# Kernel optimization log

Measured on AMD Instinct MI355X. Metric: run time of the kernel, lower is better.

The kernel has to match this reference:

```python
import jax, jax.numpy as jnp
import numpy as np

D_MODEL = 512; D_STATE = 64; D_CONV = 4; EXPAND = 2; HEADDIM = 64
D_INNER = EXPAND * D_MODEL          # 1024
NHEADS = D_INNER // HEADDIM         # 16
D_IN_PROJ = 2 * D_INNER + 2 * D_STATE + NHEADS  # z, xBC, dt
CONV_DIM = D_INNER + 2 * D_STATE
BETA = 0.5
BATCH = 8; SEQLEN = 1024
EPS_LN = 1e-12; EPS_RMS = 1e-5


def layernorm(x, w, b, eps=EPS_LN):
    mu = jnp.mean(x, axis=-1, keepdims=True)
    var = jnp.var(x, axis=-1, keepdims=True)
    return (x - mu) * jax.lax.rsqrt(var + eps) * w + b


def causal_dw_conv(x, w, b):
    # x: (b, l, c); w: (c, d_conv) depthwise; causal left-pad d_conv-1
    xt = jnp.transpose(x, (0, 2, 1))                 # (b, c, l)
    k = w[:, None, :]                                # (c, 1, d_conv)
    y = jax.lax.conv_general_dilated(
        xt, k, window_strides=(1,), padding=[(D_CONV - 1, 0)],
        feature_group_count=CONV_DIM,
        dimension_numbers=('NCH', 'OIH', 'NCH'))
    return jnp.transpose(y, (0, 2, 1)) + b


def ssd(x, dt, A, Bm, Cm, Dp):
    # x: (b,l,h,p)  dt: (b,l,h)  A: (h)  Bm,Cm: (b,l,n)  Dp: (h)
    dA = jnp.exp(dt * A)  # (b,l,h) decay per step

    def step(h, inp):
        dA_t, dt_t, B_t, C_t, x_t = inp
        # h: (b, heads, p, n)
        h = h * dA_t[:, :, None, None] + jnp.einsum('bh,bn,bhp->bhpn', dt_t, B_t, x_t)
        y = jnp.einsum('bhpn,bn->bhp', h, C_t)
        return h, y

    init = jnp.zeros((x.shape[0], NHEADS, HEADDIM, D_STATE), x.dtype)
    xs = (jnp.moveaxis(dA, 1, 0), jnp.moveaxis(dt, 1, 0),
          jnp.moveaxis(Bm, 1, 0), jnp.moveaxis(Cm, 1, 0), jnp.moveaxis(x, 1, 0))
    _, ys = jax.lax.scan(step, init, xs)
    y = jnp.moveaxis(ys, 0, 1)           # (b,l,h,p)
    return y + x * Dp[None, None, :, None]


def mamba2(u, in_proj_w, conv_w, conv_b, dt_bias, A_log, Dp, norm_w, out_proj_w):
    zxbcdt = u @ in_proj_w.T                                   # (b,l,D_IN_PROJ)
    z, xBC, dt = jnp.split(zxbcdt, [D_INNER, D_INNER + CONV_DIM], axis=-1)
    dt = jax.nn.softplus(dt + dt_bias)                          # (b,l,h)
    xBC = jax.nn.silu(causal_dw_conv(xBC, conv_w, conv_b))
    x, Bm, Cm = jnp.split(xBC, [D_INNER, D_INNER + D_STATE], axis=-1)
    x = x.reshape(x.shape[0], x.shape[1], NHEADS, HEADDIM)
    A = -jnp.exp(A_log)
    y = ssd(x, dt, A, Bm, Cm, Dp)
    y = y.reshape(y.shape[0], y.shape[1], D_INNER)
    g = y * jax.nn.silu(z)                                      # gated RMSNorm
    g = g * jax.lax.rsqrt(jnp.mean(g * g, axis=-1, keepdims=True) + EPS_RMS) * norm_w
    return g @ out_proj_w.T


def ffn(x, w1, b1, w2, b2, lnw, lnb):
    h = jax.nn.gelu(x @ w1.T + b1, approximate=False)
    h = h @ w2.T + b2
    return layernorm(h + x, lnw, lnb)


def setup_inputs() -> dict:
    key = jax.random.key(0)
    ks = jax.random.split(key, 12)
    item_emb = jax.random.normal(ks[0], (BATCH, SEQLEN, D_MODEL), jnp.float32)
    item_idx = jnp.zeros((BATCH, SEQLEN), jnp.int32)          # single sequence per row
    flip_index = jnp.arange(SEQLEN - 1, -1, -1, dtype=jnp.int64)
    s = 0.02
    in_proj_w = jax.random.normal(ks[1], (D_IN_PROJ, D_MODEL), jnp.float32) * s
    conv_w = jax.random.uniform(ks[2], (CONV_DIM, D_CONV), jnp.float32, -0.5, 0.5)
    conv_b = jnp.zeros((CONV_DIM,), jnp.float32)
    # dt_bias = inverse softplus of dt ~ U[1e-3, 0.1] in log space (mamba init)
    dt = jnp.exp(jax.random.uniform(ks[3], (NHEADS,), jnp.float32,
                                    np.log(1e-3), np.log(0.1)))
    dt_bias = dt + jnp.log(-jnp.expm1(-dt))
    A_log = jnp.log(jax.random.uniform(ks[4], (NHEADS,), jnp.float32, 1.0, 16.0))
    Dp = jnp.ones((NHEADS,), jnp.float32)
    norm_w = jnp.ones((D_INNER,), jnp.float32)
    out_proj_w = jax.random.normal(ks[5], (D_MODEL, D_INNER), jnp.float32) * s
    ln_w = jnp.ones((D_MODEL,), jnp.float32); ln_b = jnp.zeros((D_MODEL,), jnp.float32)
    ffn_w1 = jax.random.normal(ks[6], (4 * D_MODEL, D_MODEL), jnp.float32) * s
    ffn_b1 = jnp.zeros((4 * D_MODEL,), jnp.float32)
    ffn_w2 = jax.random.normal(ks[7], (D_MODEL, 4 * D_MODEL), jnp.float32) * s
    ffn_b2 = jnp.zeros((D_MODEL,), jnp.float32)
    ffn_ln_w = jnp.ones((D_MODEL,), jnp.float32); ffn_ln_b = jnp.zeros((D_MODEL,), jnp.float32)
    return dict(item_emb=item_emb, item_idx=item_idx, flip_index=flip_index,
                in_proj_w=in_proj_w, conv_w=conv_w, conv_b=conv_b, dt_bias=dt_bias,
                A_log=A_log, Dp=Dp, norm_w=norm_w, out_proj_w=out_proj_w,
                ln_w=ln_w, ln_b=ln_b, ffn_w1=ffn_w1, ffn_b1=ffn_b1,
                ffn_w2=ffn_w2, ffn_b2=ffn_b2, ffn_ln_w=ffn_ln_w, ffn_ln_b=ffn_ln_b)


def reference(item_emb, item_idx, flip_index, in_proj_w, conv_w, conv_b, dt_bias,
              A_log, Dp, norm_w, out_proj_w, ln_w, ln_b,
              ffn_w1, ffn_b1, ffn_w2, ffn_b2, ffn_ln_w, ffn_ln_b):
    # item_idx (seq_idx) is all-zeros -> no state resets; dropout is eval-mode identity.
    params = (in_proj_w, conv_w, conv_b, dt_bias, A_log, Dp, norm_w, out_proj_w)
    fwd = mamba2(item_emb, *params)
    bwd = mamba2(item_emb[:, flip_index, :], *params)   # shared weights, as in source
    h = fwd + bwd * BETA + item_emb
    h = layernorm(h, ln_w, ln_b)
    return ffn(h, ffn_w1, ffn_b1, ffn_w2, ffn_b2, ffn_ln_w, ffn_ln_b)
```

## Files before the change

kernel.cpp:

```cpp
#include <hip/hip_runtime.h>
#include <math.h>

#define SEQ     1024
#define NBATCH  8
#define NTOK    8192
#define DMODEL  512
#define DINNER  1024
#define NHEADS  16
#define DPROJ   2192
#define DPROJP  2304
#define CONVDIM 1152
#define DFFN    2048

typedef short bf16x8 __attribute__((ext_vector_type(8)));
typedef float f32x4  __attribute__((ext_vector_type(4)));

__device__ inline unsigned short f2bf(float f) {
  union { float f; unsigned int u; } v; v.f = f;
  unsigned int u = v.u;
  return (unsigned short)((u + 0x7FFFu + ((u >> 16) & 1u)) >> 16);
}
__device__ inline float bf2f(unsigned short s) {
  union { unsigned int u; float f; } v; v.u = ((unsigned int)s) << 16;
  return v.f;
}

#define GLDS16(g, l)                                                         \
  __builtin_amdgcn_global_load_lds(                                          \
      (const __attribute__((address_space(1))) unsigned int*)(g),            \
      (__attribute__((address_space(3))) unsigned int*)(l), 16, 0, 0)

__global__ __launch_bounds__(256) void cvt_bf16(const float* __restrict__ s,
                                                unsigned short* __restrict__ d, int n) {
  int i = blockIdx.x * 256 + threadIdx.x;
  if (i < n) d[i] = f2bf(s[i]);
}

__global__ __launch_bounds__(256) void cvt_bf16_pad(const float* __restrict__ s,
                                                    unsigned short* __restrict__ d,
                                                    int realrows, int cols, int padrows) {
  int i = blockIdx.x * 256 + threadIdx.x;
  if (i < padrows * cols) {
    int r = i / cols;
    d[i] = (r < realrows) ? f2bf(s[i]) : (unsigned short)0;
  }
}

template <int MODE>
__global__ __launch_bounds__(256)
void gemm_bt(const unsigned short* __restrict__ A, const unsigned short* __restrict__ B,
             void* __restrict__ Cout, const float* __restrict__ bias,
             float* __restrict__ aux, int Ksub, int lda, int Nreal, size_t zstrideC) {
  __shared__ unsigned short sA[2][128 * 32];
  __shared__ unsigned short sB[2][128 * 32];
  const int tid = threadIdx.x;
  const int bx = blockIdx.x, by = blockIdx.y, bz = blockIdx.z;
  const int lane = tid & 63;
  const int wave = tid >> 6;
  const int wm = wave >> 1, wn = wave & 1;
  const int arow = tid >> 2;
  const int acol = (tid & 3) << 3;

  const unsigned short* pA = A + (size_t)(by * 128 + arow) * lda + bz * Ksub + acol;
  const unsigned short* pB = B + (size_t)(bx * 128 + arow) * lda + bz * Ksub + acol;
  const size_t stride64 = (size_t)64 * lda;
  char* sAw[2] = { (char*)&sA[0][0] + wave * 1024, (char*)&sA[1][0] + wave * 1024 };
  char* sBw[2] = { (char*)&sB[0][0] + wave * 1024, (char*)&sB[1][0] + wave * 1024 };

  f32x4 acc[4][4];
#pragma unroll
  for (int i = 0; i < 4; i++)
#pragma unroll
    for (int j = 0; j < 4; j++) { f32x4 z = {0.f, 0.f, 0.f, 0.f}; acc[i][j] = z; }

  GLDS16(pA, sAw[0]);
  GLDS16(pA + stride64, sAw[0] + 4096);
  GLDS16(pB, sBw[0]);
  GLDS16(pB + stride64, sBw[0] + 4096);
  pA += 32; pB += 32;
  __syncthreads();

  const int lrow = lane & 15;
  const int lkq = (lane >> 4) << 3;
  int cur = 0;
  for (int k0 = 0; k0 < Ksub; k0 += 32) {
    if (k0 + 32 < Ksub) {
      const int nxt = cur ^ 1;
      GLDS16(pA, sAw[nxt]);
      GLDS16(pA + stride64, sAw[nxt] + 4096);
      GLDS16(pB, sBw[nxt]);
      GLDS16(pB + stride64, sBw[nxt] + 4096);
      pA += 32; pB += 32;
    }
    bf16x8 af[4], bfr[4];
#pragma unroll
    for (int mi = 0; mi < 4; mi++)
      af[mi] = *(const bf16x8*)&sA[cur][(wm * 64 + mi * 16 + lrow) * 32 + lkq];
#pragma unroll
    for (int ni = 0; ni < 4; ni++)
      bfr[ni] = *(const bf16x8*)&sB[cur][(wn * 64 + ni * 16 + lrow) * 32 + lkq];
#pragma unroll
    for (int mi = 0; mi < 4; mi++)
#pragma unroll
      for (int ni = 0; ni < 4; ni++)
        acc[mi][ni] = __builtin_amdgcn_mfma_f32_16x16x32_bf16(af[mi], bfr[ni], acc[mi][ni], 0, 0, 0);
    __syncthreads();
    cur ^= 1;
  }

  const int row0 = by * 128 + wm * 64;
  const int col0 = bx * 128 + wn * 64;
  float* outf = (float*)Cout;
  unsigned short* outp16 = (unsigned short*)Cout + (size_t)bz * zstrideC;
#pragma unroll
  for (int mi = 0; mi < 4; mi++) {
#pragma unroll
    for (int ni = 0; ni < 4; ni++) {
      const int col = col0 + ni * 16 + lrow;
      if (col < Nreal) {
        const float bval = (MODE == 0 || MODE == 1) && bias ? bias[col] : 0.f;
#pragma unroll
        for (int r = 0; r < 4; r++) {
          const int row = row0 + mi * 16 + ((lane >> 4) << 2) + r;
          float v = acc[mi][ni][r] + bval;
          if (MODE == 1) {
            float g = 0.5f * v * (1.f + erff(v * 0.7071067811865476f));
            ((unsigned short*)Cout)[(size_t)row * Nreal + col] = f2bf(g);
          } else if (MODE == 2) {
            ((unsigned short*)Cout)[(size_t)row * Nreal + col] = f2bf(v);
            if (col >= 2176) aux[(size_t)row * 16 + (col - 2176)] = v;
          } else if (MODE == 3) {
            outp16[(size_t)row * Nreal + col] = f2bf(v);
          } else {
            outf[(size_t)row * Nreal + col] = v;
          }
        }
      }
    }
  }
}

__global__ __launch_bounds__(256)
void dt_softplus(const float* __restrict__ zdt, const float* __restrict__ dt_bias,
                 float* __restrict__ dtf, float* __restrict__ dtb) {
  int i = blockIdx.x * 256 + threadIdx.x;
  int dir = i >> 17;
  int rem = i & 131071;
  int row = rem >> 10;
  int t = rem & 1023;
  int b = row >> 4, h = row & 15;
  int srow = (b << 10) + (dir ? (1023 - t) : t);
  float v = zdt[(size_t)srow * 16 + h] + dt_bias[h];
  float dt = (v > 20.f) ? v : log1pf(expf(v));
  (dir ? dtb : dtf)[(row << 10) + t] = dt;
}

__global__ __launch_bounds__(256)
void conv_silu_bf(const unsigned short* __restrict__ zxb, const float* __restrict__ cw,
                  const float* __restrict__ cb,
                  unsigned short* __restrict__ xcf, unsigned short* __restrict__ xcb) {
  const int tid = threadIdx.x;
  const int c = blockIdx.x * 128 + (tid & 127);
  const int b = blockIdx.y;
  const int seg = blockIdx.z * 2 + (tid >> 7);
  const int t0 = seg << 5;
  const float w0 = cw[c * 4 + 0], w1 = cw[c * 4 + 1], w2 = cw[c * 4 + 2], w3 = cw[c * 4 + 3];
  const float bias = cb[c];
  const unsigned short* src = zxb + (size_t)(b << 10) * DPROJ + DINNER + c;
  unsigned short* dstf = xcf + (size_t)(b << 10) * CONVDIM + c;
  unsigned short* dstb = xcb + (size_t)(b << 10) * CONVDIM + c;
  float r0 = 0.f, r1 = 0.f, r2 = 0.f;
  if (t0 >= 3) {
    r0 = bf2f(src[(size_t)(t0 - 3) * DPROJ]);
    r1 = bf2f(src[(size_t)(t0 - 2) * DPROJ]);
    r2 = bf2f(src[(size_t)(t0 - 1) * DPROJ]);
  }
  for (int s = t0; s < t0 + 32; s++) {
    float x = bf2f(src[(size_t)s * DPROJ]);
    float vf = bias + w0 * r0 + w1 * r1 + w2 * r2 + w3 * x;
    dstf[(size_t)s * CONVDIM] = f2bf(vf / (1.f + expf(-vf)));
    int tp = 1026 - s;
    if (tp <= 1023) {
      float vb = bias + w0 * x + w1 * r2 + w2 * r1 + w3 * r0;
      dstb[(size_t)tp * CONVDIM] = f2bf(vb / (1.f + expf(-vb)));
    }
    r0 = r1; r1 = r2; r2 = x;
  }
  if (seg == 31) {
    float v2 = bias + w1 * r2 + w2 * r1 + w3 * r0;
    float v1 = bias + w2 * r2 + w3 * r1;
    float v0 = bias + w3 * r2;
    dstb[(size_t)2 * CONVDIM] = f2bf(v2 / (1.f + expf(-v2)));
    dstb[(size_t)1 * CONVDIM] = f2bf(v1 / (1.f + expf(-v1)));
    dstb[0] = f2bf(v0 / (1.f + expf(-v0)));
  }
}

__global__ __launch_bounds__(512)
void ssd_chunk(const unsigned short* __restrict__ xcf, const unsigned short* __restrict__ xcb,
               const float* __restrict__ dtf, const float* __restrict__ dtb,
               const float* __restrict__ A_log, const float* __restrict__ Dp,
               unsigned short* __restrict__ yf, unsigned short* __restrict__ yb) {
  const int blk = blockIdx.x;
  const int dir = blk >> 7;
  const int b = (blk >> 4) & 7;
  const int h = blk & 15;
  const unsigned short* xc = dir ? xcb : xcf;
  const float* dts = (dir ? dtb : dtf) + ((size_t)((b << 4) + h) << 10);
  unsigned short* yo = dir ? yb : yf;
  const float A = -expf(A_log[h]);
  const float Dh = Dp[h];
  const int tid = threadIdx.x;
  const int lane = tid & 63;
  const int w = tid >> 6;
  const int wm = w >> 1;
  const int wn = w & 1;
  const int lrow = lane & 15;
  const int quad = lane >> 4;
  const int lk8 = quad << 3;
  const int bS = b << 10;

  __shared__ unsigned short Cb[2][64 * 72];
  __shared__ unsigned short Bb[2][64 * 72];
  __shared__ unsigned short Xt[2][64 * 72];
  __shared__ unsigned short Bt[2][64 * 72];
  __shared__ unsigned short Hb[2][64 * 72];
  __shared__ unsigned short Mb[64 * 72];
  __shared__ float sdt_all[1024];
  __shared__ float Lv_all[16][64];
  __shared__ float ev_all[16][64];
  __shared__ float wv_all[16][64];
  __shared__ float dtot_all[16];

  const unsigned short* bcrow = xc + (size_t)(bS + (tid >> 3)) * CONVDIM + (tid & 7) * 8;
  const int pr = tid & 31;
  const int sg = tid >> 5;
  const unsigned short* trow = xc + (size_t)(bS + sg * 4) * CONVDIM;

  uint4 vb, vc;
  unsigned int xv[4], bv[4];

  vb = *(const uint4*)(bcrow + 1024);
  vc = *(const uint4*)(bcrow + 1088);
  {
    const unsigned short* tp = trow;
#pragma unroll
    for (int k = 0; k < 4; k++) {
      xv[k] = *(const unsigned int*)(tp + h * 64 + pr * 2);
      bv[k] = *(const unsigned int*)(tp + 1024 + pr * 2);
      tp += CONVDIM;
    }
  }

  *(float2*)&sdt_all[tid * 2] = *(const float2*)(dts + tid * 2);
  {
    uint4 z; z.x = 0u; z.y = 0u; z.z = 0u; z.w = 0u;
    *(uint4*)&Hb[0][(tid >> 3) * 72 + (tid & 7) * 8] = z;
  }
  __syncthreads();

#pragma unroll
  for (int r = 0; r < 2; r++) {
    const int c = w * 2 + r;
    float dtl = sdt_all[c * 64 + lane];
    float v = dtl;
#pragma unroll
    for (int off = 1; off < 64; off <<= 1) {
      float o = __shfl_up(v, off);
      if (lane >= off) v += o;
    }
    const float Lv = A * v;
    const float LL = __shfl(Lv, 63);
    Lv_all[c][lane] = Lv;
    ev_all[c][lane] = expf(Lv);
    wv_all[c][lane] = dtl * expf(LL - Lv);
    if (lane == 0) dtot_all[c] = expf(LL);
  }
  __syncthreads();

  auto stage_write = [&](int buf, int c) {
    *(uint4*)&Bb[buf][(tid >> 3) * 72 + (tid & 7) * 8] = vb;
    *(uint4*)&Cb[buf][(tid >> 3) * 72 + (tid & 7) * 8] = vc;
    unsigned short x0[4], x1[4], b0[4], b1[4];
#pragma unroll
    for (int k = 0; k < 4; k++) {
      float ws = wv_all[c][sg * 4 + k];
      x0[k] = (unsigned short)(xv[k] & 0xffff);
      x1[k] = (unsigned short)(xv[k] >> 16);
      b0[k] = f2bf(bf2f((unsigned short)(bv[k] & 0xffff)) * ws);
      b1[k] = f2bf(bf2f((unsigned short)(bv[k] >> 16)) * ws);
    }
    *(uint2*)&Xt[buf][(pr * 2 + 0) * 72 + sg * 4] = *(const uint2*)x0;
    *(uint2*)&Xt[buf][(pr * 2 + 1) * 72 + sg * 4] = *(const uint2*)x1;
    *(uint2*)&Bt[buf][(pr * 2 + 0) * 72 + sg * 4] = *(const uint2*)b0;
    *(uint2*)&Bt[buf][(pr * 2 + 1) * 72 + sg * 4] = *(const uint2*)b1;
  };
  auto stage_load = [&](int c) {
    const unsigned short* rp = bcrow + (size_t)c * 64 * CONVDIM;
    vb = *(const uint4*)(rp + 1024);
    vc = *(const uint4*)(rp + 1088);
    const unsigned short* tp = trow + (size_t)c * 64 * CONVDIM;
#pragma unroll
    for (int k = 0; k < 4; k++) {
      xv[k] = *(const unsigned int*)(tp + h * 64 + pr * 2);
      bv[k] = *(const unsigned int*)(tp + 1024 + pr * 2);
      tp += CONVDIM;
    }
  };

  stage_write(0, 0);
  stage_load(1);
  __syncthreads();

  f32x4 hacc[2];
#pragma unroll
  for (int j = 0; j < 2; j++) { f32x4 z = {0.f, 0.f, 0.f, 0.f}; hacc[j] = z; }

  int cur = 0;
  for (int c = 0; c < 16; c++) {
    const int t0 = c << 6;

    f32x4 m1[2];
#pragma unroll
    for (int j = 0; j < 2; j++) { f32x4 z = {0.f, 0.f, 0.f, 0.f}; m1[j] = z; }
#pragma unroll
    for (int kq = 0; kq < 2; kq++) {
      bf16x8 af = *(const bf16x8*)&Cb[cur][(wm * 16 + lrow) * 72 + kq * 32 + lk8];
#pragma unroll
      for (int j = 0; j < 2; j++) {
        bf16x8 bf = *(const bf16x8*)&Bb[cur][(wn * 32 + j * 16 + lrow) * 72 + kq * 32 + lk8];
        m1[j] = __builtin_amdgcn_mfma_f32_16x16x32_bf16(af, bf, m1[j], 0, 0, 0);
      }
    }
#pragma unroll
    for (int r = 0; r < 4; r++) {
      const int i = wm * 16 + quad * 4 + r;
      const float Li = Lv_all[c][i];
#pragma unroll
      for (int j = 0; j < 2; j++) {
        const int s = wn * 32 + j * 16 + lrow;
        const float Ls = Lv_all[c][s];
        const float ds = sdt_all[c * 64 + s];
        float val = (s <= i) ? m1[j][r] * expf(Li - Ls) * ds : 0.f;
        Mb[i * 72 + s] = f2bf(val);
      }
    }
    __syncthreads();

    f32x4 Y[2], T[2], S[2];
#pragma unroll
    for (int j = 0; j < 2; j++) {
      f32x4 z = {0.f, 0.f, 0.f, 0.f};
      Y[j] = z; T[j] = z; S[j] = z;
    }
#pragma unroll
    for (int kq = 0; kq < 2; kq++) {
      bf16x8 am = *(const bf16x8*)&Mb[(wm * 16 + lrow) * 72 + kq * 32 + lk8];
      bf16x8 ac = *(const bf16x8*)&Cb[cur][(wm * 16 + lrow) * 72 + kq * 32 + lk8];
      bf16x8 ax = *(const bf16x8*)&Xt[cur][(wm * 16 + lrow) * 72 + kq * 32 + lk8];
#pragma unroll
      for (int j = 0; j < 2; j++) {
        const int brow = (wn * 32 + j * 16 + lrow) * 72 + kq * 32 + lk8;
        bf16x8 bx = *(const bf16x8*)&Xt[cur][brow];
        bf16x8 bh = *(const bf16x8*)&Hb[cur][brow];
        bf16x8 bw = *(const bf16x8*)&Bt[cur][brow];
        Y[j] = __builtin_amdgcn_mfma_f32_16x16x32_bf16(am, bx, Y[j], 0, 0, 0);
        T[j] = __builtin_amdgcn_mfma_f32_16x16x32_bf16(ac, bh, T[j], 0, 0, 0);
        S[j] = __builtin_amdgcn_mfma_f32_16x16x32_bf16(ax, bw, S[j], 0, 0, 0);
      }
    }

    const float dtot = dtot_all[c];
#pragma unroll
    for (int r = 0; r < 4; r++) {
      const int i = wm * 16 + quad * 4 + r;
      const float ei = ev_all[c][i];
#pragma unroll
      for (int j = 0; j < 2; j++) {
        const int p = wn * 32 + j * 16 + lrow;
        float yv = Y[j][r] + ei * T[j][r] + Dh * bf2f(Xt[cur][p * 72 + i]);
        yo[(size_t)(bS + t0 + i) * DINNER + h * 64 + p] = f2bf(yv);
      }
    }
#pragma unroll
    for (int j = 0; j < 2; j++)
#pragma unroll
      for (int r = 0; r < 4; r++)
        hacc[j][r] = dtot * hacc[j][r] + S[j][r];

    const int nxt = cur ^ 1;
    if (c + 1 < 16) {
#pragma unroll
      for (int j = 0; j < 2; j++)
#pragma unroll
        for (int r = 0; r < 4; r++)
          Hb[nxt][(wm * 16 + quad * 4 + r) * 72 + wn * 32 + j * 16 + lrow] = f2bf(hacc[j][r]);
      stage_write(nxt, c + 1);
      if (c + 2 < 16) stage_load(c + 2);
    }
    __syncthreads();
    cur = nxt;
  }
}

__device__ inline float2 block_sum2_256(float a, float b) {
#pragma unroll
  for (int o = 32; o >= 1; o >>= 1) { a += __shfl_xor(a, o); b += __shfl_xor(b, o); }
  __shared__ float ra[4], rb[4];
  const int lane = threadIdx.x & 63, w = threadIdx.x >> 6;
  if (lane == 0) { ra[w] = a; rb[w] = b; }
  __syncthreads();
  float2 out;
  out.x = ra[0] + ra[1] + ra[2] + ra[3];
  out.y = rb[0] + rb[1] + rb[2] + rb[3];
  return out;
}

__global__ __launch_bounds__(256)
void gate_rms_comb(const unsigned short* __restrict__ yf, const unsigned short* __restrict__ yb,
                   const unsigned short* __restrict__ zxb, const float* __restrict__ nw,
                   unsigned short* __restrict__ comb) {
  const int bt = blockIdx.x;
  const int b = bt >> 10, t = bt & 1023;
  const int zrowb = (b << 10) + (1023 - t);
  const int tid = threadIdx.x;
  ushort4 yf4 = *(const ushort4*)(yf + (size_t)bt * DINNER + tid * 4);
  ushort4 yb4 = *(const ushort4*)(yb + (size_t)bt * DINNER + tid * 4);
  ushort4 zf4 = *(const ushort4*)(zxb + (size_t)bt * DPROJ + tid * 4);
  ushort4 zb4 = *(const ushort4*)(zxb + (size_t)zrowb * DPROJ + tid * 4);
  float gf[4], gb[4];
  {
    float z0 = bf2f(zf4.x), z1 = bf2f(zf4.y), z2 = bf2f(zf4.z), z3 = bf2f(zf4.w);
    gf[0] = bf2f(yf4.x) * (z0 / (1.f + expf(-z0)));
    gf[1] = bf2f(yf4.y) * (z1 / (1.f + expf(-z1)));
    gf[2] = bf2f(yf4.z) * (z2 / (1.f + expf(-z2)));
    gf[3] = bf2f(yf4.w) * (z3 / (1.f + expf(-z3)));
  }
  {
    float z0 = bf2f(zb4.x), z1 = bf2f(zb4.y), z2 = bf2f(zb4.z), z3 = bf2f(zb4.w);
    gb[0] = bf2f(yb4.x) * (z0 / (1.f + expf(-z0)));
    gb[1] = bf2f(yb4.y) * (z1 / (1.f + expf(-z1)));
    gb[2] = bf2f(yb4.z) * (z2 / (1.f + expf(-z2)));
    gb[3] = bf2f(yb4.w) * (z3 / (1.f + expf(-z3)));
  }
  float2 sr = block_sum2_256(gf[0]*gf[0] + gf[1]*gf[1] + gf[2]*gf[2] + gf[3]*gf[3],
                             gb[0]*gb[0] + gb[1]*gb[1] + gb[2]*gb[2] + gb[3]*gb[3]);
  float sf = rsqrtf(sr.x * (1.f / 1024.f) + 1e-5f);
  float sb = 0.5f * rsqrtf(sr.y * (1.f / 1024.f) + 1e-5f);
  float4 wv = *(const float4*)(nw + tid * 4);
  unsigned short* o = comb + (size_t)bt * DINNER + tid * 4;
  o[0] = f2bf((gf[0] * sf + gb[0] * sb) * wv.x);
  o[1] = f2bf((gf[1] * sf + gb[1] * sb) * wv.y);
  o[2] = f2bf((gf[2] * sf + gb[2] * sb) * wv.z);
  o[3] = f2bf((gf[3] * sf + gb[3] * sb) * wv.w);
}

__global__ __launch_bounds__(256)
void combine_ln(const unsigned short* __restrict__ mo, const float* __restrict__ u,
                const float* __restrict__ w, const float* __restrict__ bias,
                float* __restrict__ hln, unsigned short* __restrict__ hbf) {
  const int bt = blockIdx.x;
  const int tid = threadIdx.x;
  const float2 uu = *(const float2*)(u + (size_t)bt * DMODEL + tid * 2);
  float vx = uu.x, vy = uu.y;
#pragma unroll
  for (int z = 0; z < 4; z++) {
    ushort2 p = *(const ushort2*)(mo + (size_t)z * NTOK * DMODEL + (size_t)bt * DMODEL + tid * 2);
    vx += bf2f(p.x);
    vy += bf2f(p.y);
  }
  float2 sr = block_sum2_256(vx + vy, vx * vx + vy * vy);
  float mean = sr.x * (1.f / 512.f);
  float var = sr.y * (1.f / 512.f) - mean * mean;
  float inv = rsqrtf(var + 1e-12f);
  float2 wv = *(const float2*)(w + tid * 2);
  float2 bv = *(const float2*)(bias + tid * 2);
  float ox = (vx - mean) * inv * wv.x + bv.x;
  float oy = (vy - mean) * inv * wv.y + bv.y;
  *(float2*)(hln + (size_t)bt * DMODEL + tid * 2) = make_float2(ox, oy);
  hbf[(size_t)bt * DMODEL + tid * 2] = f2bf(ox);
  hbf[(size_t)bt * DMODEL + tid * 2 + 1] = f2bf(oy);
}

__global__ __launch_bounds__(256)
void final_ln(const unsigned short* __restrict__ f2, const float* __restrict__ b2,
              const float* __restrict__ hln,
              const float* __restrict__ w, const float* __restrict__ bias,
              float* __restrict__ outp) {
  const int bt = blockIdx.x;
  const int tid = threadIdx.x;
  const float2 bb = *(const float2*)(b2 + tid * 2);
  const float2 h = *(const float2*)(hln + (size_t)bt * DMODEL + tid * 2);
  float vx = bb.x + h.x;
  float vy = bb.y + h.y;
#pragma unroll
  for (int z = 0; z < 4; z++) {
    ushort2 p = *(const ushort2*)(f2 + (size_t)z * NTOK * DMODEL + (size_t)bt * DMODEL + tid * 2);
    vx += bf2f(p.x);
    vy += bf2f(p.y);
  }
  float2 sr = block_sum2_256(vx + vy, vx * vx + vy * vy);
  float mean = sr.x * (1.f / 512.f);
  float var = sr.y * (1.f / 512.f) - mean * mean;
  float inv = rsqrtf(var + 1e-12f);
  float2 wv = *(const float2*)(w + tid * 2);
  float2 bv = *(const float2*)(bias + tid * 2);
  *(float2*)(outp + (size_t)bt * DMODEL + tid * 2) =
      make_float2((vx - mean) * inv * wv.x + bv.x, (vy - mean) * inv * wv.y + bv.y);
}

extern "C" void kernel_launch(void* const* d_in, const int* in_sizes, int n_in,
                              void* d_out, int out_size, void* d_ws, size_t ws_size,
                              hipStream_t stream) {
  const float* item_emb   = (const float*)d_in[0];
  const float* in_proj_w  = (const float*)d_in[3];
  const float* conv_w     = (const float*)d_in[4];
  const float* conv_b     = (const float*)d_in[5];
  const float* dt_bias    = (const float*)d_in[6];
  const float* A_log      = (const float*)d_in[7];
  const float* Dp         = (const float*)d_in[8];
  const float* norm_w     = (const float*)d_in[9];
  const float* out_proj_w = (const float*)d_in[10];
  const float* ln_w       = (const float*)d_in[11];
  const float* ln_b       = (const float*)d_in[12];
  const float* w1         = (const float*)d_in[13];
  const float* b1         = (const float*)d_in[14];
  const float* w2         = (const float*)d_in[15];
  const float* b2         = (const float*)d_in[16];
  const float* fln_w      = (const float*)d_in[17];
  const float* fln_b      = (const float*)d_in[18];
  float* outp = (float*)d_out;
  char* ws = (char*)d_ws;

  const size_t o_ubf  = 0;
  const size_t o_win  = 8388608;
  const size_t o_wout = 10747904;
  const size_t o_w1   = 11796480;
  const size_t o_w2   = 13893632;
  const size_t o_dtf  = 15990784;
  const size_t o_dtb  = 16515072;
  const size_t o_zdt  = 17039360;
  const size_t o_zxb  = 17563648;
  const size_t o_xcf  = 53477376;
  const size_t o_xcb  = 72351744;
  const size_t o_yf   = 91226112;
  const size_t o_yb   = 108003328;
  const size_t o_comb = o_xcf;
  const size_t o_mo   = o_zxb;
  const size_t o_hln  = o_yb;
  const size_t o_hbf  = o_ubf;
  const size_t o_h1   = o_xcb;
  const size_t o_f2   = o_zxb;

  unsigned short* u_bf  = (unsigned short*)(ws + o_ubf);
  unsigned short* winb  = (unsigned short*)(ws + o_win);
  unsigned short* woutb = (unsigned short*)(ws + o_wout);
  unsigned short* w1b   = (unsigned short*)(ws + o_w1);
  unsigned short* w2b   = (unsigned short*)(ws + o_w2);
  float* dtf = (float*)(ws + o_dtf);
  float* dtb = (float*)(ws + o_dtb);
  float* zdt = (float*)(ws + o_zdt);
  unsigned short* zxb = (unsigned short*)(ws + o_zxb);
  unsigned short* xcf = (unsigned short*)(ws + o_xcf);
  unsigned short* xcb = (unsigned short*)(ws + o_xcb);
  unsigned short* yf  = (unsigned short*)(ws + o_yf);
  unsigned short* yb  = (unsigned short*)(ws + o_yb);
  unsigned short* comb = (unsigned short*)(ws + o_comb);
  unsigned short* mo  = (unsigned short*)(ws + o_mo);
  float* hln = (float*)(ws + o_hln);
  unsigned short* hbf = (unsigned short*)(ws + o_hbf);
  unsigned short* h1b = (unsigned short*)(ws + o_h1);
  unsigned short* f2  = (unsigned short*)(ws + o_f2);

  {
    int n = NTOK * DMODEL;
    cvt_bf16<<<(n + 255) / 256, 256, 0, stream>>>(item_emb, u_bf, n);
    cvt_bf16_pad<<<(DPROJP * DMODEL + 255) / 256, 256, 0, stream>>>(in_proj_w, winb, DPROJ, DMODEL, DPROJP);
    n = DMODEL * DINNER;
    cvt_bf16<<<(n + 255) / 256, 256, 0, stream>>>(out_proj_w, woutb, n);
    n = DFFN * DMODEL;
    cvt_bf16<<<(n + 255) / 256, 256, 0, stream>>>(w1, w1b, n);
    n = DMODEL * DFFN;
    cvt_bf16<<<(n + 255) / 256, 256, 0, stream>>>(w2, w2b, n);
  }

  gemm_bt<2><<<dim3(DPROJP / 128, NTOK / 128), 256, 0, stream>>>(
      u_bf, winb, zxb, nullptr, zdt, DMODEL, DMODEL, DPROJ, 0);

  dt_softplus<<<1024, 256, 0, stream>>>(zdt, dt_bias, dtf, dtb);
  conv_silu_bf<<<dim3(9, NBATCH, 16), 256, 0, stream>>>(zxb, conv_w, conv_b, xcf, xcb);

  ssd_chunk<<<256, 512, 0, stream>>>(xcf, xcb, dtf, dtb, A_log, Dp, yf, yb);

  gate_rms_comb<<<NTOK, 256, 0, stream>>>(yf, yb, zxb, norm_w, comb);

  gemm_bt<3><<<dim3(DMODEL / 128, NTOK / 128, 4), 256, 0, stream>>>(
      comb, woutb, mo, nullptr, nullptr, DINNER / 4, DINNER, DMODEL,
      (size_t)NTOK * DMODEL);

  combine_ln<<<NTOK, 256, 0, stream>>>(mo, item_emb, ln_w, ln_b, hln, hbf);

  gemm_bt<1><<<dim3(DFFN / 128, NTOK / 128), 256, 0, stream>>>(
      hbf, w1b, h1b, b1, nullptr, DMODEL, DMODEL, DFFN, 0);

  gemm_bt<3><<<dim3(DMODEL / 128, NTOK / 128, 4), 256, 0, stream>>>(
      h1b, w2b, f2, nullptr, nullptr, DFFN / 4, DFFN, DMODEL,
      (size_t)NTOK * DMODEL);

  final_ln<<<NTOK, 256, 0, stream>>>(f2, b2, hln, fln_w, fln_b, outp);

  (void)in_sizes; (void)n_in; (void)out_size; (void)ws_size;
}
```

Before: 365.6 us.

## Triple-buffer GEMM LDS tiles with explicit vmcnt waits and raw barriers

Moves the bf16 GEMM's shared-memory staging from two buffers to three. Global-to-LDS loads are now issued two K-steps ahead, and the code waits with partial vmcnt counts plus s_barrier instead of a full __syncthreads each iteration. The aim is to hide global load latency and avoid draining all outstanding memory operations every step. In exchange, LDS use per block grows by half, which may lower occupancy. Correctness also now relies on the hand-written vmcnt counts matching the compiler's actual instruction stream.

```diff
diff --git a/kernel.cpp b/kernel.cpp
--- a/kernel.cpp
+++ b/kernel.cpp
@@ -51,8 +51,8 @@
 void gemm_bt(const unsigned short* __restrict__ A, const unsigned short* __restrict__ B,
              void* __restrict__ Cout, const float* __restrict__ bias,
              float* __restrict__ aux, int Ksub, int lda, int Nreal, size_t zstrideC) {
-  __shared__ unsigned short sA[2][128 * 32];
-  __shared__ unsigned short sB[2][128 * 32];
+  __shared__ unsigned short sA[3][128 * 32];
+  __shared__ unsigned short sB[3][128 * 32];
   const int tid = threadIdx.x;
   const int bx = blockIdx.x, by = blockIdx.y, bz = blockIdx.z;
   const int lane = tid & 63;
@@ -61,11 +61,9 @@
   const int arow = tid >> 2;
   const int acol = (tid & 3) << 3;
 
-  const unsigned short* pA = A + (size_t)(by * 128 + arow) * lda + bz * Ksub + acol;
-  const unsigned short* pB = B + (size_t)(bx * 128 + arow) * lda + bz * Ksub + acol;
+  const unsigned short* pA0 = A + (size_t)(by * 128 + arow) * lda + bz * Ksub + acol;
+  const unsigned short* pB0 = B + (size_t)(bx * 128 + arow) * lda + bz * Ksub + acol;
   const size_t stride64 = (size_t)64 * lda;
-  char* sAw[2] = { (char*)&sA[0][0] + wave * 1024, (char*)&sA[1][0] + wave * 1024 };
-  char* sBw[2] = { (char*)&sB[0][0] + wave * 1024, (char*)&sB[1][0] + wave * 1024 };
 
   f32x4 acc[4][4];
 #pragma unroll
@@ -73,25 +71,33 @@
 #pragma unroll
     for (int j = 0; j < 4; j++) { f32x4 z = {0.f, 0.f, 0.f, 0.f}; acc[i][j] = z; }
 
-  GLDS16(pA, sAw[0]);
-  GLDS16(pA + stride64, sAw[0] + 4096);
-  GLDS16(pB, sBw[0]);
-  GLDS16(pB + stride64, sBw[0] + 4096);
-  pA += 32; pB += 32;
-  __syncthreads();
+  auto stage = [&](int kk) {
+    const int bsel = kk % 3;
+    const unsigned short* a = pA0 + kk * 32;
+    const unsigned short* b = pB0 + kk * 32;
+    char* la = (char*)&sA[bsel][0] + wave * 1024;
+    char* lb = (char*)&sB[bsel][0] + wave * 1024;
+    GLDS16(a, la);
+    GLDS16(a + stride64, la + 4096);
+    GLDS16(b, lb);
+    GLDS16(b + stride64, lb + 4096);
+  };
+
+  const int nk = Ksub >> 5;
+  stage(0);
+  if (nk > 1) {
+    stage(1);
+    asm volatile("s_waitcnt vmcnt(4)" ::: "memory");
+  } else {
+    asm volatile("s_waitcnt vmcnt(0)" ::: "memory");
+  }
+  __builtin_amdgcn_s_barrier();
 
   const int lrow = lane & 15;
   const int lkq = (lane >> 4) << 3;
-  int cur = 0;
-  for (int k0 = 0; k0 < Ksub; k0 += 32) {
-    if (k0 + 32 < Ksub) {
-      const int nxt = cur ^ 1;
-      GLDS16(pA, sAw[nxt]);
-      GLDS16(pA + stride64, sAw[nxt] + 4096);
-      GLDS16(pB, sBw[nxt]);
-      GLDS16(pB + stride64, sBw[nxt] + 4096);
-      pA += 32; pB += 32;
-    }
+  for (int k = 0; k < nk; ++k) {
+    if (k + 2 < nk) stage(k + 2);
+    const int cur = k % 3;
     bf16x8 af[4], bfr[4];
 #pragma unroll
     for (int mi = 0; mi < 4; mi++)
@@ -104,8 +110,12 @@
 #pragma unroll
       for (int ni = 0; ni < 4; ni++)
         acc[mi][ni] = __builtin_amdgcn_mfma_f32_16x16x32_bf16(af[mi], bfr[ni], acc[mi][ni], 0, 0, 0);
-    __syncthreads();
-    cur ^= 1;
+    if (k + 2 < nk) {
+      asm volatile("s_waitcnt vmcnt(4)" ::: "memory");
+    } else if (k + 1 < nk) {
+      asm volatile("s_waitcnt vmcnt(0)" ::: "memory");
+    }
+    if (k + 1 < nk) __builtin_amdgcn_s_barrier();
   }
 
   const int row0 = by * 128 + wm * 64;
```

Result: no change. 372.0 us (+1.8%).

## Enlarge GEMM tiles to 256x128, fuse dt softplus into in_proj epilogue, merge weight casts

Applied to the files above, without the earlier changes.

GEMM blocks now use 512 threads computing 256x128 output tiles, doubling reuse of each staged B tile and halving block count. The softplus on dt is computed directly in the in_proj GEMM epilogue and written in both forward and reversed layouts, removing a separate kernel and intermediate buffer. The four weight bf16 conversions are merged into one launch. Larger tiles increase LDS use and reduce the number of blocks, which may hurt occupancy or wave balance.

```diff
diff --git a/kernel.cpp b/kernel.cpp
--- a/kernel.cpp
+++ b/kernel.cpp
@@ -36,22 +36,34 @@
   if (i < n) d[i] = f2bf(s[i]);
 }
 
-__global__ __launch_bounds__(256) void cvt_bf16_pad(const float* __restrict__ s,
-                                                    unsigned short* __restrict__ d,
-                                                    int realrows, int cols, int padrows) {
+__global__ __launch_bounds__(256)
+void cvt_weights(const float* __restrict__ inw, const float* __restrict__ outw,
+                 const float* __restrict__ w1, const float* __restrict__ w2,
+                 unsigned short* __restrict__ winb, unsigned short* __restrict__ woutb,
+                 unsigned short* __restrict__ w1b, unsigned short* __restrict__ w2b) {
   int i = blockIdx.x * 256 + threadIdx.x;
-  if (i < padrows * cols) {
-    int r = i / cols;
-    d[i] = (r < realrows) ? f2bf(s[i]) : (unsigned short)0;
+  const int n0 = DPROJP * DMODEL;
+  const int n1 = DMODEL * DINNER;
+  const int n2 = DFFN * DMODEL;
+  const int n3 = DMODEL * DFFN;
+  if (i < n0) {
+    int r = i / DMODEL;
+    winb[i] = (r < DPROJ) ? f2bf(inw[i]) : (unsigned short)0;
+  } else if ((i -= n0) < n1) {
+    woutb[i] = f2bf(outw[i]);
+  } else if ((i -= n1) < n2) {
+    w1b[i] = f2bf(w1[i]);
+  } else if ((i -= n2) < n3) {
+    w2b[i] = f2bf(w2[i]);
   }
 }
 
 template <int MODE>
-__global__ __launch_bounds__(256)
+__global__ __launch_bounds__(512)
 void gemm_bt(const unsigned short* __restrict__ A, const unsigned short* __restrict__ B,
              void* __restrict__ Cout, const float* __restrict__ bias,
              float* __restrict__ aux, int Ksub, int lda, int Nreal, size_t zstrideC) {
-  __shared__ unsigned short sA[2][128 * 32];
+  __shared__ unsigned short sA[2][256 * 32];
   __shared__ unsigned short sB[2][128 * 32];
   const int tid = threadIdx.x;
   const int bx = blockIdx.x, by = blockIdx.y, bz = blockIdx.z;
@@ -61,11 +73,9 @@
   const int arow = tid >> 2;
   const int acol = (tid & 3) << 3;
 
-  const unsigned short* pA = A + (size_t)(by * 128 + arow) * lda + bz * Ksub + acol;
-  const unsigned short* pB = B + (size_t)(bx * 128 + arow) * lda + bz * Ksub + acol;
-  const size_t stride64 = (size_t)64 * lda;
-  char* sAw[2] = { (char*)&sA[0][0] + wave * 1024, (char*)&sA[1][0] + wave * 1024 };
-  char* sBw[2] = { (char*)&sB[0][0] + wave * 1024, (char*)&sB[1][0] + wave * 1024 };
+  const unsigned short* pA0 = A + (size_t)(by * 256 + arow) * lda + bz * Ksub + acol;
+  const unsigned short* pB0 = B + (size_t)(bx * 128 + arow) * lda + bz * Ksub + acol;
+  const size_t stride128 = (size_t)128 * lda;
 
   f32x4 acc[4][4];
 #pragma unroll
@@ -73,25 +83,25 @@
 #pragma unroll
     for (int j = 0; j < 4; j++) { f32x4 z = {0.f, 0.f, 0.f, 0.f}; acc[i][j] = z; }
 
-  GLDS16(pA, sAw[0]);
-  GLDS16(pA + stride64, sAw[0] + 4096);
-  GLDS16(pB, sBw[0]);
-  GLDS16(pB + stride64, sBw[0] + 4096);
-  pA += 32; pB += 32;
+  auto stage = [&](int kk, int buf) {
+    const unsigned short* a = pA0 + kk * 32;
+    const unsigned short* b = pB0 + kk * 32;
+    char* la = (char*)&sA[buf][0] + wave * 1024;
+    char* lb = (char*)&sB[buf][0] + wave * 1024;
+    GLDS16(a, la);
+    GLDS16(a + stride128, la + 8192);
+    GLDS16(b, lb);
+  };
+
+  const int nk = Ksub >> 5;
+  stage(0, 0);
   __syncthreads();
 
   const int lrow = lane & 15;
   const int lkq = (lane >> 4) << 3;
   int cur = 0;
-  for (int k0 = 0; k0 < Ksub; k0 += 32) {
-    if (k0 + 32 < Ksub) {
-      const int nxt = cur ^ 1;
-      GLDS16(pA, sAw[nxt]);
-      GLDS16(pA + stride64, sAw[nxt] + 4096);
-      GLDS16(pB, sBw[nxt]);
-      GLDS16(pB + stride64, sBw[nxt] + 4096);
-      pA += 32; pB += 32;
-    }
+  for (int k = 0; k < nk; ++k) {
+    if (k + 1 < nk) stage(k + 1, cur ^ 1);
     bf16x8 af[4], bfr[4];
 #pragma unroll
     for (int mi = 0; mi < 4; mi++)
@@ -108,7 +118,7 @@
     cur ^= 1;
   }
 
-  const int row0 = by * 128 + wm * 64;
+  const int row0 = by * 256 + wm * 64;
   const int col0 = bx * 128 + wn * 64;
   float* outf = (float*)Cout;
   unsigned short* outp16 = (unsigned short*)Cout + (size_t)bz * zstrideC;
@@ -128,7 +138,15 @@
             ((unsigned short*)Cout)[(size_t)row * Nreal + col] = f2bf(g);
           } else if (MODE == 2) {
             ((unsigned short*)Cout)[(size_t)row * Nreal + col] = f2bf(v);
-            if (col >= 2176) aux[(size_t)row * 16 + (col - 2176)] = v;
+            if (col >= 2176) {
+              const int hh = col - 2176;
+              const float vv = v + bias[hh];
+              const float dtv = (vv > 20.f) ? vv : log1pf(expf(vv));
+              const int bb = row >> 10, tt = row & 1023;
+              const size_t rr = (size_t)((bb << 4) + hh) << 10;
+              aux[rr + tt] = dtv;
+              aux[131072 + rr + (1023 - tt)] = dtv;
+            }
           } else if (MODE == 3) {
             outp16[(size_t)row * Nreal + col] = f2bf(v);
           } else {
@@ -138,21 +156,6 @@
       }
     }
   }
-}
-
-__global__ __launch_bounds__(256)
-void dt_softplus(const float* __restrict__ zdt, const float* __restrict__ dt_bias,
-                 float* __restrict__ dtf, float* __restrict__ dtb) {
-  int i = blockIdx.x * 256 + threadIdx.x;
-  int dir = i >> 17;
-  int rem = i & 131071;
-  int row = rem >> 10;
-  int t = rem & 1023;
-  int b = row >> 4, h = row & 15;
-  int srow = (b << 10) + (dir ? (1023 - t) : t);
-  float v = zdt[(size_t)srow * 16 + h] + dt_bias[h];
-  float dt = (v > 20.f) ? v : log1pf(expf(v));
-  (dir ? dtb : dtf)[(row << 10) + t] = dt;
 }
 
 __global__ __launch_bounds__(256)
@@ -539,7 +542,6 @@
   const size_t o_w2   = 13893632;
   const size_t o_dtf  = 15990784;
   const size_t o_dtb  = 16515072;
-  const size_t o_zdt  = 17039360;
   const size_t o_zxb  = 17563648;
   const size_t o_xcf  = 53477376;
   const size_t o_xcb  = 72351744;
@@ -559,7 +561,6 @@
   unsigned short* w2b   = (unsigned short*)(ws + o_w2);
   float* dtf = (float*)(ws + o_dtf);
   float* dtb = (float*)(ws + o_dtb);
-  float* zdt = (float*)(ws + o_zdt);
   unsigned short* zxb = (unsigned short*)(ws + o_zxb);
   unsigned short* xcf = (unsigned short*)(ws + o_xcf);
   unsigned short* xcb = (unsigned short*)(ws + o_xcb);
@@ -575,35 +576,30 @@
   {
     int n = NTOK * DMODEL;
     cvt_bf16<<<(n + 255) / 256, 256, 0, stream>>>(item_emb, u_bf, n);
-    cvt_bf16_pad<<<(DPROJP * DMODEL + 255) / 256, 256, 0, stream>>>(in_proj_w, winb, DPROJ, DMODEL, DPROJP);
-    n = DMODEL * DINNER;
-    cvt_bf16<<<(n + 255) / 256, 256, 0, stream>>>(out_proj_w, woutb, n);
-    n = DFFN * DMODEL;
-    cvt_bf16<<<(n + 255) / 256, 256, 0, stream>>>(w1, w1b, n);
-    n = DMODEL * DFFN;
-    cvt_bf16<<<(n + 255) / 256, 256, 0, stream>>>(w2, w2b, n);
-  }
-
-  gemm_bt<2><<<dim3(DPROJP / 128, NTOK / 128), 256, 0, stream>>>(
-      u_bf, winb, zxb, nullptr, zdt, DMODEL, DMODEL, DPROJ, 0);
-
-  dt_softplus<<<1024, 256, 0, stream>>>(zdt, dt_bias, dtf, dtb);
+    int nw = DPROJP * DMODEL + DMODEL * DINNER + DFFN * DMODEL + DMODEL * DFFN;
+    cvt_weights<<<(nw + 255) / 256, 256, 0, stream>>>(in_proj_w, out_proj_w, w1, w2,
+                                                      winb, woutb, w1b, w2b);
+  }
+
+  gemm_bt<2><<<dim3(DPROJP / 128, NTOK / 256), 512, 0, stream>>>(
+      u_bf, winb, zxb, dt_bias, dtf, DMODEL, DMODEL, DPROJ, 0);
+
   conv_silu_bf<<<dim3(9, NBATCH, 16), 256, 0, stream>>>(zxb, conv_w, conv_b, xcf, xcb);
 
   ssd_chunk<<<256, 512, 0, stream>>>(xcf, xcb, dtf, dtb, A_log, Dp, yf, yb);
 
   gate_rms_comb<<<NTOK, 256, 0, stream>>>(yf, yb, zxb, norm_w, comb);
 
-  gemm_bt<3><<<dim3(DMODEL / 128, NTOK / 128, 4), 256, 0, stream>>>(
+  gemm_bt<3><<<dim3(DMODEL / 128, NTOK / 256, 4), 512, 0, stream>>>(
       comb, woutb, mo, nullptr, nullptr, DINNER / 4, DINNER, DMODEL,
       (size_t)NTOK * DMODEL);
 
   combine_ln<<<NTOK, 256, 0, stream>>>(mo, item_emb, ln_w, ln_b, hln, hbf);
 
-  gemm_bt<1><<<dim3(DFFN / 128, NTOK / 128), 256, 0, stream>>>(
+  gemm_bt<1><<<dim3(DFFN / 128, NTOK / 256), 512, 0, stream>>>(
       hbf, w1b, h1b, b1, nullptr, DMODEL, DMODEL, DFFN, 0);
 
-  gemm_bt<3><<<dim3(DMODEL / 128, NTOK / 128, 4), 256, 0, stream>>>(
+  gemm_bt<3><<<dim3(DMODEL / 128, NTOK / 256, 4), 512, 0, stream>>>(
       h1b, w2b, f2, nullptr, nullptr, DFFN / 4, DFFN, DMODEL,
       (size_t)NTOK * DMODEL);
 
```

Result: no change. 370.8 us (+1.4%).

## Fuse x-channel causal conv+SiLU into SSD chunk kernel; merge weight conversions

Applied to the files above, without the earlier changes.

The depthwise conv and SiLU for the 1024 x channels now run inside the SSD chunk kernel, computed straight from the in-projection output with a 7-row halo per thread. Only the B/C channels (128) still go through a separate conv kernel into a compact buffer. This drops the write and re-read of the full conv output for x in both directions, at the cost of redundant halo loads and extra exp work inside the SSD kernel's staging path. The four weight bf16 conversion launches are also merged into one kernel to cut launch overhead.

```diff
diff --git a/kernel.cpp b/kernel.cpp
--- a/kernel.cpp
+++ b/kernel.cpp
@@ -36,13 +36,25 @@
   if (i < n) d[i] = f2bf(s[i]);
 }
 
-__global__ __launch_bounds__(256) void cvt_bf16_pad(const float* __restrict__ s,
-                                                    unsigned short* __restrict__ d,
-                                                    int realrows, int cols, int padrows) {
+__global__ __launch_bounds__(256)
+void cvt_weights(const float* __restrict__ inw, const float* __restrict__ outw,
+                 const float* __restrict__ w1, const float* __restrict__ w2,
+                 unsigned short* __restrict__ winb, unsigned short* __restrict__ woutb,
+                 unsigned short* __restrict__ w1b, unsigned short* __restrict__ w2b) {
   int i = blockIdx.x * 256 + threadIdx.x;
-  if (i < padrows * cols) {
-    int r = i / cols;
-    d[i] = (r < realrows) ? f2bf(s[i]) : (unsigned short)0;
+  const int n0 = DPROJP * DMODEL;
+  const int n1 = DMODEL * DINNER;
+  const int n2 = DFFN * DMODEL;
+  const int n3 = DMODEL * DFFN;
+  if (i < n0) {
+    int r = i / DMODEL;
+    winb[i] = (r < DPROJ) ? f2bf(inw[i]) : (unsigned short)0;
+  } else if ((i -= n0) < n1) {
+    woutb[i] = f2bf(outw[i]);
+  } else if ((i -= n1) < n2) {
+    w1b[i] = f2bf(w1[i]);
+  } else if ((i -= n2) < n3) {
+    w2b[i] = f2bf(w2[i]);
   }
 }
 
@@ -156,19 +168,20 @@
 }
 
 __global__ __launch_bounds__(256)
-void conv_silu_bf(const unsigned short* __restrict__ zxb, const float* __restrict__ cw,
-                  const float* __restrict__ cb,
-                  unsigned short* __restrict__ xcf, unsigned short* __restrict__ xcb) {
+void conv_bc(const unsigned short* __restrict__ zxb, const float* __restrict__ cw,
+             const float* __restrict__ cb,
+             unsigned short* __restrict__ xbcf, unsigned short* __restrict__ xbcb) {
   const int tid = threadIdx.x;
-  const int c = blockIdx.x * 128 + (tid & 127);
+  const int c128 = tid & 127;
+  const int c = 1024 + c128;
   const int b = blockIdx.y;
-  const int seg = blockIdx.z * 2 + (tid >> 7);
+  const int seg = blockIdx.x * 2 + (tid >> 7);
   const int t0 = seg << 5;
   const float w0 = cw[c * 4 + 0], w1 = cw[c * 4 + 1], w2 = cw[c * 4 + 2], w3 = cw[c * 4 + 3];
   const float bias = cb[c];
   const unsigned short* src = zxb + (size_t)(b << 10) * DPROJ + DINNER + c;
-  unsigned short* dstf = xcf + (size_t)(b << 10) * CONVDIM + c;
-  unsigned short* dstb = xcb + (size_t)(b << 10) * CONVDIM + c;
+  unsigned short* dstf = xbcf + (size_t)(b << 10) * 128 + c128;
+  unsigned short* dstb = xbcb + (size_t)(b << 10) * 128 + c128;
   float r0 = 0.f, r1 = 0.f, r2 = 0.f;
   if (t0 >= 3) {
     r0 = bf2f(src[(size_t)(t0 - 3) * DPROJ]);
@@ -178,11 +191,11 @@
   for (int s = t0; s < t0 + 32; s++) {
     float x = bf2f(src[(size_t)s * DPROJ]);
     float vf = bias + w0 * r0 + w1 * r1 + w2 * r2 + w3 * x;
-    dstf[(size_t)s * CONVDIM] = f2bf(vf / (1.f + expf(-vf)));
+    dstf[(size_t)s * 128] = f2bf(vf / (1.f + expf(-vf)));
     int tp = 1026 - s;
     if (tp <= 1023) {
       float vb = bias + w0 * x + w1 * r2 + w2 * r1 + w3 * r0;
-      dstb[(size_t)tp * CONVDIM] = f2bf(vb / (1.f + expf(-vb)));
+      dstb[(size_t)tp * 128] = f2bf(vb / (1.f + expf(-vb)));
     }
     r0 = r1; r1 = r2; r2 = x;
   }
@@ -190,14 +203,16 @@
     float v2 = bias + w1 * r2 + w2 * r1 + w3 * r0;
     float v1 = bias + w2 * r2 + w3 * r1;
     float v0 = bias + w3 * r2;
-    dstb[(size_t)2 * CONVDIM] = f2bf(v2 / (1.f + expf(-v2)));
-    dstb[(size_t)1 * CONVDIM] = f2bf(v1 / (1.f + expf(-v1)));
+    dstb[(size_t)2 * 128] = f2bf(v2 / (1.f + expf(-v2)));
+    dstb[(size_t)1 * 128] = f2bf(v1 / (1.f + expf(-v1)));
     dstb[0] = f2bf(v0 / (1.f + expf(-v0)));
   }
 }
 
 __global__ __launch_bounds__(512)
-void ssd_chunk(const unsigned short* __restrict__ xcf, const unsigned short* __restrict__ xcb,
+void ssd_chunk(const unsigned short* __restrict__ zxb,
+               const unsigned short* __restrict__ xbcf, const unsigned short* __restrict__ xbcb,
+               const float* __restrict__ cw, const float* __restrict__ cb,
                const float* __restrict__ dtf, const float* __restrict__ dtb,
                const float* __restrict__ A_log, const float* __restrict__ Dp,
                unsigned short* __restrict__ yf, unsigned short* __restrict__ yb) {
@@ -205,7 +220,7 @@
   const int dir = blk >> 7;
   const int b = (blk >> 4) & 7;
   const int h = blk & 15;
-  const unsigned short* xc = dir ? xcb : xcf;
+  const unsigned short* xbc = dir ? xbcb : xbcf;
   const float* dts = (dir ? dtb : dtf) + ((size_t)((b << 4) + h) << 10);
   unsigned short* yo = dir ? yb : yf;
   const float A = -expf(A_log[h]);
@@ -232,25 +247,64 @@
   __shared__ float wv_all[16][64];
   __shared__ float dtot_all[16];
 
-  const unsigned short* bcrow = xc + (size_t)(bS + (tid >> 3)) * CONVDIM + (tid & 7) * 8;
+  const unsigned short* bcrow = xbc + (size_t)(bS + (tid >> 3)) * 128 + (tid & 7) * 8;
   const int pr = tid & 31;
   const int sg = tid >> 5;
-  const unsigned short* trow = xc + (size_t)(bS + sg * 4) * CONVDIM;
+  const int ccx = h * 64 + pr * 2;
+  const unsigned short* bvrow = xbc + (size_t)(bS + sg * 4) * 128 + pr * 2;
+  const float4 wx0 = *(const float4*)(cw + ccx * 4);
+  const float4 wx1 = *(const float4*)(cw + (ccx + 1) * 4);
+  const float bx0 = cb[ccx], bx1 = cb[ccx + 1];
 
   uint4 vb, vc;
-  unsigned int xv[4], bv[4];
-
-  vb = *(const uint4*)(bcrow + 1024);
-  vc = *(const uint4*)(bcrow + 1088);
-  {
-    const unsigned short* tp = trow;
+  unsigned int bv[4];
+  unsigned int xin[7];
+
+  auto stage_load = [&](int c) {
+    const unsigned short* rp = bcrow + (size_t)c * 64 * 128;
+    vb = *(const uint4*)(rp);
+    vc = *(const uint4*)(rp + 64);
+    const unsigned short* tp = bvrow + (size_t)c * 64 * 128;
+#pragma unroll
+    for (int k = 0; k < 4; k++) bv[k] = *(const unsigned int*)(tp + (size_t)k * 128);
+    const int li0 = c * 64 + sg * 4 - 3;
+#pragma unroll
+    for (int j = 0; j < 7; j++) {
+      const int li = li0 + j;
+      const int g = dir ? (1023 - li) : li;
+      xin[j] = (g >= 0 && g < 1024)
+               ? *(const unsigned int*)(zxb + (size_t)(bS + g) * DPROJ + DINNER + ccx)
+               : 0u;
+    }
+  };
+
+  auto stage_write = [&](int buf, int c) {
+    *(uint4*)&Bb[buf][(tid >> 3) * 72 + (tid & 7) * 8] = vb;
+    *(uint4*)&Cb[buf][(tid >> 3) * 72 + (tid & 7) * 8] = vc;
+    float f0[7], f1[7];
+#pragma unroll
+    for (int j = 0; j < 7; j++) {
+      f0[j] = bf2f((unsigned short)(xin[j] & 0xffff));
+      f1[j] = bf2f((unsigned short)(xin[j] >> 16));
+    }
+    unsigned short x0[4], x1[4], b0[4], b1[4];
 #pragma unroll
     for (int k = 0; k < 4; k++) {
-      xv[k] = *(const unsigned int*)(tp + h * 64 + pr * 2);
-      bv[k] = *(const unsigned int*)(tp + 1024 + pr * 2);
-      tp += CONVDIM;
-    }
-  }
+      const float ws = wv_all[c][sg * 4 + k];
+      float v0 = bx0 + wx0.x * f0[k] + wx0.y * f0[k + 1] + wx0.z * f0[k + 2] + wx0.w * f0[k + 3];
+      float v1 = bx1 + wx1.x * f1[k] + wx1.y * f1[k + 1] + wx1.z * f1[k + 2] + wx1.w * f1[k + 3];
+      x0[k] = f2bf(v0 / (1.f + expf(-v0)));
+      x1[k] = f2bf(v1 / (1.f + expf(-v1)));
+      b0[k] = f2bf(bf2f((unsigned short)(bv[k] & 0xffff)) * ws);
+      b1[k] = f2bf(bf2f((unsigned short)(bv[k] >> 16)) * ws);
+    }
+    *(uint2*)&Xt[buf][(pr * 2 + 0) * 72 + sg * 4] = *(const uint2*)x0;
+    *(uint2*)&Xt[buf][(pr * 2 + 1) * 72 + sg * 4] = *(const uint2*)x1;
+    *(uint2*)&Bt[buf][(pr * 2 + 0) * 72 + sg * 4] = *(const uint2*)b0;
+    *(uint2*)&Bt[buf][(pr * 2 + 1) * 72 + sg * 4] = *(const uint2*)b1;
+  };
+
+  stage_load(0);
 
   *(float2*)&sdt_all[tid * 2] = *(const float2*)(dts + tid * 2);
   {
@@ -277,36 +331,6 @@
     if (lane == 0) dtot_all[c] = expf(LL);
   }
   __syncthreads();
-
-  auto stage_write = [&](int buf, int c) {
-    *(uint4*)&Bb[buf][(tid >> 3) * 72 + (tid & 7) * 8] = vb;
-    *(uint4*)&Cb[buf][(tid >> 3) * 72 + (tid & 7) * 8] = vc;
-    unsigned short x0[4], x1[4], b0[4], b1[4];
-#pragma unroll
-    for (int k = 0; k < 4; k++) {
-      float ws = wv_all[c][sg * 4 + k];
-      x0[k] = (unsigned short)(xv[k] & 0xffff);
-      x1[k] = (unsigned short)(xv[k] >> 16);
-      b0[k] = f2bf(bf2f((unsigned short)(bv[k] & 0xffff)) * ws);
-      b1[k] = f2bf(bf2f((unsigned short)(bv[k] >> 16)) * ws);
-    }
-    *(uint2*)&Xt[buf][(pr * 2 + 0) * 72 + sg * 4] = *(const uint2*)x0;
-    *(uint2*)&Xt[buf][(pr * 2 + 1) * 72 + sg * 4] = *(const uint2*)x1;
-    *(uint2*)&Bt[buf][(pr * 2 + 0) * 72 + sg * 4] = *(const uint2*)b0;
-    *(uint2*)&Bt[buf][(pr * 2 + 1) * 72 + sg * 4] = *(const uint2*)b1;
-  };
-  auto stage_load = [&](int c) {
-    const unsigned short* rp = bcrow + (size_t)c * 64 * CONVDIM;
-    vb = *(const uint4*)(rp + 1024);
-    vc = *(const uint4*)(rp + 1088);
-    const unsigned short* tp = trow + (size_t)c * 64 * CONVDIM;
-#pragma unroll
-    for (int k = 0; k < 4; k++) {
-      xv[k] = *(const unsigned int*)(tp + h * 64 + pr * 2);
-      bv[k] = *(const unsigned int*)(tp + 1024 + pr * 2);
-      tp += CONVDIM;
-    }
-  };
 
   stage_write(0, 0);
   stage_load(1);
@@ -542,14 +566,15 @@
   const size_t o_zdt  = 17039360;
   const size_t o_zxb  = 17563648;
   const size_t o_xcf  = 53477376;
-  const size_t o_xcb  = 72351744;
+  const size_t o_xbcf = 72351744;
+  const size_t o_xbcb = 74448896;
   const size_t o_yf   = 91226112;
   const size_t o_yb   = 108003328;
   const size_t o_comb = o_xcf;
   const size_t o_mo   = o_zxb;
   const size_t o_hln  = o_yb;
   const size_t o_hbf  = o_ubf;
-  const size_t o_h1   = o_xcb;
+  const size_t o_h1   = o_xbcf;
   const size_t o_f2   = o_zxb;
 
   unsigned short* u_bf  = (unsigned short*)(ws + o_ubf);
@@ -560,9 +585,9 @@
   float* dtf = (float*)(ws + o_dtf);
   float* dtb = (float*)(ws + o_dtb);
   float* zdt = (float*)(ws + o_zdt);
-  unsigned short* zxb = (unsigned short*)(ws + o_zxb);
-  unsigned short* xcf = (unsigned short*)(ws + o_xcf);
-  unsigned short* xcb = (unsigned short*)(ws + o_xcb);
+  unsigned short* zxb  = (unsigned short*)(ws + o_zxb);
+  unsigned short* xbcf = (unsigned short*)(ws + o_xbcf);
+  unsigned short* xbcb = (unsigned short*)(ws + o_xbcb);
   unsigned short* yf  = (unsigned short*)(ws + o_yf);
   unsigned short* yb  = (unsigned short*)(ws + o_yb);
   unsigned short* comb = (unsigned short*)(ws + o_comb);
@@ -575,22 +600,19 @@
   {
     int n = NTOK * DMODEL;
     cvt_bf16<<<(n + 255) / 256, 256, 0, stream>>>(item_emb, u_bf, n);
-    cvt_bf16_pad<<<(DPROJP * DMODEL + 255) / 256, 256, 0, stream>>>(in_proj_w, winb, DPROJ, DMODEL, DPROJP);
-    n = DMODEL * DINNER;
-    cvt_bf16<<<(n + 255) / 256, 256, 0, stream>>>(out_proj_w, woutb, n);
-    n = DFFN * DMODEL;
-    cvt_bf16<<<(n + 255) / 256, 256, 0, stream>>>(w1, w1b, n);
-    n = DMODEL * DFFN;
-    cvt_bf16<<<(n + 255) / 256, 256, 0, stream>>>(w2, w2b, n);
+    int nw = DPROJP * DMODEL + DMODEL * DINNER + DFFN * DMODEL + DMODEL * DFFN;
+    cvt_weights<<<(nw + 255) / 256, 256, 0, stream>>>(in_proj_w, out_proj_w, w1, w2,
+                                                      winb, woutb, w1b, w2b);
   }
 
   gemm_bt<2><<<dim3(DPROJP / 128, NTOK / 128), 256, 0, stream>>>(
       u_bf, winb, zxb, nullptr, zdt, DMODEL, DMODEL, DPROJ, 0);
 
   dt_softplus<<<1024, 256, 0, stream>>>(zdt, dt_bias, dtf, dtb);
-  conv_silu_bf<<<dim3(9, NBATCH, 16), 256, 0, stream>>>(zxb, conv_w, conv_b, xcf, xcb);
-
-  ssd_chunk<<<256, 512, 0, stream>>>(xcf, xcb, dtf, dtb, A_log, Dp, yf, yb);
+  conv_bc<<<dim3(16, NBATCH), 256, 0, stream>>>(zxb, conv_w, conv_b, xbcf, xbcb);
+
+  ssd_chunk<<<256, 512, 0, stream>>>(zxb, xbcf, xbcb, conv_w, conv_b,
+                                     dtf, dtb, A_log, Dp, yf, yb);
 
   gate_rms_comb<<<NTOK, 256, 0, stream>>>(yf, yb, zxb, norm_w, comb);
 
```

Result: no change. 365.8 us (+0.1%).
